# Kernel optimization log

Measured on AMD Instinct MI355X. Metric: run time of the kernel, lower is better.

Reference implementation:

```python
import jax, jax.numpy as jnp
import numpy as np


def gcn_conv(x, W, b, src, dst, dinv_sqrt, n_nodes):
    # PyG GCNConv: h = X W; out_i = sum_j norm_ij * h_j + b, norm = d_i^-1/2 d_j^-1/2
    h = x @ W  # [N, out]
    norm = dinv_sqrt[src] * dinv_sqrt[dst]  # [E]
    msg = h[src] * norm[:, None]  # [E, out]
    out = jax.ops.segment_sum(msg, dst, num_segments=n_nodes)
    return out + b


def setup_inputs() -> dict:
    key = jax.random.key(0)
    ks = jax.random.split(key, 12)
    N, E, G = 50000, 400000, 512
    x = jax.random.normal(ks[0], (N, 3), dtype=jnp.float32)
    edge_index = jax.random.randint(ks[1], (2, E), 0, N, dtype=jnp.int64)
    batch = jnp.sort(jax.random.randint(ks[2], (N,), 0, G, dtype=jnp.int64))
    def lin(k, fin, fout):
        kw, kb = jax.random.split(k)
        s = 1.0 / np.sqrt(fin)
        return (jax.random.uniform(kw, (fin, fout), jnp.float32, -s, s),
                jax.random.uniform(kb, (fout,), jnp.float32, -s, s))
    W1, b1 = lin(ks[3], 3, 100)
    W2, b2 = lin(ks[4], 100, 200)
    W3, b3 = lin(ks[5], 200, 100)
    W4, b4 = lin(ks[6], 100, 1)
    return {"x": x, "edge_index": edge_index, "batch": batch, "num_graphs": G,
            "W1": W1, "b1": b1, "W2": W2, "b2": b2,
            "W3": W3, "b3": b3, "W4": W4, "b4": b4}


def reference(x, edge_index, batch, num_graphs, W1, b1, W2, b2, W3, b3, W4, b4):
    N = x.shape[0]
    loop = jnp.arange(N, dtype=edge_index.dtype)
    src = jnp.concatenate([edge_index[0], loop])  # self-loops added (GCNConv default)
    dst = jnp.concatenate([edge_index[1], loop])
    deg = jax.ops.segment_sum(jnp.ones_like(src, dtype=x.dtype), dst, num_segments=N)
    dinv_sqrt = deg ** -0.5  # deg >= 1 due to self-loops

    h = jax.nn.silu(gcn_conv(x, W1, b1, src, dst, dinv_sqrt, N))
    h = jax.nn.silu(gcn_conv(h, W2, b2, src, dst, dinv_sqrt, N))

    # global_mean_pool over `batch` segments
    sums = jax.ops.segment_sum(h, batch, num_segments=num_graphs)  # [G, 200]
    cnts = jax.ops.segment_sum(jnp.ones((N,), h.dtype), batch, num_segments=num_graphs)
    pooled = sums / jnp.maximum(cnts, 1.0)[:, None]

    h = jax.nn.silu(pooled @ W3 + b3)
    out = h @ W4 + b4  # [G, 1]
    return out.squeeze(-1)
```

## Files before the change

### kernel.cpp

```cpp
#include <hip/hip_runtime.h>
#include <math.h>

#define WF 64

__device__ __forceinline__ float silu_f(float v){
  float e = __builtin_amdgcn_exp2f(v * -1.44269504088896340736f);
  return v * __builtin_amdgcn_rcpf(1.0f + e);
}

typedef __attribute__((ext_vector_type(8))) short bf16x8;
typedef __attribute__((ext_vector_type(4))) float f32x4;

__device__ __forceinline__ void bf16split(float v, unsigned short& h, unsigned short& l){
  unsigned int b = __float_as_uint(v);
  unsigned int hh = (b + 0x8000u) >> 16;
  float hf = __uint_as_float(hh << 16);
  float lo = v - hf;
  unsigned int bl = __float_as_uint(lo);
  h = (unsigned short)hh;
  l = (unsigned short)((bl + 0x8000u) >> 16);
}

__global__ __launch_bounds__(256) void k_count(const int* __restrict__ dst, int* __restrict__ cnt, int E){
  int e = blockIdx.x*blockDim.x + threadIdx.x;
  if (e < E) atomicAdd(&cnt[dst[e]], 1);
}

__global__ __launch_bounds__(256) void k_scan1(const int* __restrict__ cnt, int* __restrict__ rowstart, int* __restrict__ bsum, int N){
  __shared__ int s[256];
  int tid = threadIdx.x;
  int base = blockIdx.x*2048 + tid*8;
  int loc[8]; int tsum = 0;
#pragma unroll
  for (int j=0;j<8;++j){ int idx=base+j; int v = (idx<N)?cnt[idx]:0; loc[j]=tsum; tsum+=v; }
  s[tid]=tsum; __syncthreads();
  for (int off=1; off<256; off<<=1){
    int v = (tid>=off)? s[tid-off] : 0;
    __syncthreads();
    s[tid] += v;
    __syncthreads();
  }
  int texc = s[tid] - tsum;
  if (tid==255) bsum[blockIdx.x] = s[255];
#pragma unroll
  for (int j=0;j<8;++j){ int idx=base+j; if (idx<N) rowstart[idx] = texc + loc[j]; }
}

__global__ __launch_bounds__(256) void k_scan3(const int* __restrict__ bsum, const int* __restrict__ cnt,
                        const float* __restrict__ x,
                        int* __restrict__ rowstart, int* __restrict__ cursor,
                        float4* __restrict__ dxp,
                        int N, int E, int nb){
  __shared__ int boffs;
  int tid = threadIdx.x;
  int b = (blockIdx.x*blockDim.x) >> 11;
  if (tid < WF){
    int v = (tid < nb && tid < b) ? bsum[tid] : 0;
#pragma unroll
    for (int off=32; off; off>>=1) v += __shfl_down(v, off);
    if (tid==0) boffs = v;
  }
  __syncthreads();
  int idx = blockIdx.x*blockDim.x + tid;
  if (idx < N){
    int v = rowstart[idx] + boffs;
    rowstart[idx]=v; cursor[idx]=v;
    float di = rsqrtf((float)(cnt[idx]+1));
    float4 o;
    o.x = di;
    o.y = di*x[3*idx+0];
    o.z = di*x[3*idx+1];
    o.w = di*x[3*idx+2];
    dxp[idx] = o;
  }
  if (idx==0) rowstart[N]=E;
}

__global__ __launch_bounds__(256) void k_fill(const int* __restrict__ src, const int* __restrict__ dst,
                       int* __restrict__ cursor, int* __restrict__ colsrc, int E){
  int e = blockIdx.x*blockDim.x + threadIdx.x;
  if (e < E){
    int d = dst[e];
    int pos = atomicAdd(&cursor[d], 1);
    colsrc[pos] = src[e];
  }
}

__global__ __launch_bounds__(256) void k_wconv(const float* __restrict__ W2,
                       unsigned short* __restrict__ w2th, unsigned short* __restrict__ w2tl){
  int idx = blockIdx.x*blockDim.x + threadIdx.x;
  if (idx < 224*128){
    int f = idx >> 7, k = idx & 127;
    float v = (f < 200 && k < 100) ? W2[(size_t)k*200 + f] : 0.f;
    unsigned short h, l;
    bf16split(v, h, l);
    w2th[idx] = h;
    w2tl[idx] = l;
  }
}

__global__ __launch_bounds__(256) void k_z1(const float4* __restrict__ dxp,
                     const int* __restrict__ rowstart, const int* __restrict__ colsrc,
                     float4* __restrict__ z1, int N){
  int i = blockIdx.x*blockDim.x + threadIdx.x;
  if (i >= N) return;
  float4 self = dxp[i];
  float di = self.x;
  float sx = self.y, sy = self.z, sz = self.w;
  int jb = rowstart[i], je = rowstart[i+1];
  int j = jb;
  for (; j+3 < je; j += 4){
    float4 r0 = dxp[colsrc[j]];
    float4 r1 = dxp[colsrc[j+1]];
    float4 r2 = dxp[colsrc[j+2]];
    float4 r3 = dxp[colsrc[j+3]];
    sx += (r0.y + r1.y) + (r2.y + r3.y);
    sy += (r0.z + r1.z) + (r2.z + r3.z);
    sz += (r0.w + r1.w) + (r2.w + r3.w);
  }
  for (; j < je; ++j){
    float4 r = dxp[colsrc[j]];
    sx += r.y; sy += r.z; sz += r.w;
  }
  float4 o;
  o.x = di;
  o.y = di*sx; o.z = di*sy; o.w = di*sz;
  z1[i] = o;
}

__global__ __launch_bounds__(256) void k_agg2f(const float4* __restrict__ z1,
                       const int* __restrict__ rowstart, const int* __restrict__ colsrc,
                       const float* __restrict__ W1, const float* __restrict__ b1,
                       unsigned short* __restrict__ a2h, unsigned short* __restrict__ a2l, int N){
  __shared__ float w[300];
  __shared__ float bb[100];
  int tid = threadIdx.x;
  for (int t=tid; t<300; t+=256) w[t]=W1[t];
  for (int t=tid; t<100; t+=256) bb[t]=b1[t];
  __syncthreads();

  int node = blockIdx.x*8 + (tid >> 5);
  int lane = tid & 31;
  if (node >= N) return;
  if (lane >= 25){
    int ko = 100 + (lane-25)*4;
    ushort4 z = make_ushort4(0,0,0,0);
    *(ushort4*)(a2h + (size_t)node*128 + ko) = z;
    *(ushort4*)(a2l + (size_t)node*128 + ko) = z;
    return;
  }
  int f0 = lane*4;
  float w0[4], w1[4], w2[4], b[4];
#pragma unroll
  for (int j=0;j<4;++j){
    w0[j] = w[f0+j]; w1[j] = w[100+f0+j]; w2[j] = w[200+f0+j]; b[j] = bb[f0+j];
  }

  float4 zn = z1[node];
  float din = zn.x;
  float acc[4];
#pragma unroll
  for (int j=0;j<4;++j){
    float h = silu_f(zn.y*w0[j] + zn.z*w1[j] + zn.w*w2[j] + b[j]);
    acc[j] = din*h;
  }
  int jb = rowstart[node], je = rowstart[node+1];
  int e = jb;
  for (; e+1 < je; e += 2){
    float4 zu0 = z1[colsrc[e]];
    float4 zu1 = z1[colsrc[e+1]];
#pragma unroll
    for (int j=0;j<4;++j){
      float h0 = silu_f(zu0.y*w0[j] + zu0.z*w1[j] + zu0.w*w2[j] + b[j]);
      float h1v = silu_f(zu1.y*w0[j] + zu1.z*w1[j] + zu1.w*w2[j] + b[j]);
      acc[j] += zu0.x*h0 + zu1.x*h1v;
    }
  }
  if (e < je){
    float4 zu = z1[colsrc[e]];
#pragma unroll
    for (int j=0;j<4;++j){
      float h = silu_f(zu.y*w0[j] + zu.z*w1[j] + zu.w*w2[j] + b[j]);
      acc[j] += zu.x*h;
    }
  }
  ushort4 h4, l4;
  bf16split(din*acc[0], h4.x, l4.x);
  bf16split(din*acc[1], h4.y, l4.y);
  bf16split(din*acc[2], h4.z, l4.z);
  bf16split(din*acc[3], h4.w, l4.w);
  *(ushort4*)(a2h + (size_t)node*128 + f0) = h4;
  *(ushort4*)(a2l + (size_t)node*128 + f0) = l4;
}

__global__ __launch_bounds__(128) void k_mm2(const unsigned short* __restrict__ a2h,
                      const unsigned short* __restrict__ a2l,
                      const unsigned short* __restrict__ w2th,
                      const unsigned short* __restrict__ w2tl,
                      const float* __restrict__ b2, const int* __restrict__ batch,
                      float* __restrict__ pooled, int N, int nwg){
  __shared__ float plL[256];
  int tid = threadIdx.x;
  int l = tid & 63, w = tid >> 6;
  int orig = blockIdx.x;
  int q = nwg >> 3, r = nwg & 7;
  int xcd = orig % 8, rk = orig / 8;
  int bid = (xcd < r) ? (xcd*(q+1) + rk) : (r*(q+1) + (xcd-r)*q + rk);
  int n0 = bid * 32;
  int row = l & 15;
  int kg  = l >> 4;

  const unsigned short* ah_p = a2h + (size_t)(n0 + w*16 + row)*128;
  const unsigned short* al_p = a2l + (size_t)(n0 + w*16 + row)*128;

  bf16x8 ahf[4], alf[4];
#pragma unroll
  for (int ks = 0; ks < 4; ++ks){
    int ko = ks*32 + kg*8;
    ahf[ks] = *(const bf16x8*)(ah_p + ko);
    alf[ks] = *(const bf16x8*)(al_p + ko);
  }

  int g0 = batch[n0];

  for (int fb = 0; fb < 7; ++fb){
    int gf0 = fb*32 + row, gf1 = gf0 + 16;
    const unsigned short* wh0_p = w2th + (size_t)gf0*128;
    const unsigned short* wl0_p = w2tl + (size_t)gf0*128;
    const unsigned short* wh1_p = w2th + (size_t)gf1*128;
    const unsigned short* wl1_p = w2tl + (size_t)gf1*128;

    f32x4 acc0 = {0.f,0.f,0.f,0.f};
    f32x4 acc1 = {0.f,0.f,0.f,0.f};
#pragma unroll
    for (int ks = 0; ks < 4; ++ks){
      int ko = ks*32 + kg*8;
      bf16x8 wh0 = *(const bf16x8*)(wh0_p + ko);
      bf16x8 wl0 = *(const bf16x8*)(wl0_p + ko);
      bf16x8 wh1 = *(const bf16x8*)(wh1_p + ko);
      bf16x8 wl1 = *(const bf16x8*)(wl1_p + ko);
      acc0 = __builtin_amdgcn_mfma_f32_16x16x32_bf16(ahf[ks], wh0, acc0, 0, 0, 0);
      acc0 = __builtin_amdgcn_mfma_f32_16x16x32_bf16(ahf[ks], wl0, acc0, 0, 0, 0);
      acc0 = __builtin_amdgcn_mfma_f32_16x16x32_bf16(alf[ks], wh0, acc0, 0, 0, 0);
      acc1 = __builtin_amdgcn_mfma_f32_16x16x32_bf16(ahf[ks], wh1, acc1, 0, 0, 0);
      acc1 = __builtin_amdgcn_mfma_f32_16x16x32_bf16(ahf[ks], wl1, acc1, 0, 0, 0);
      acc1 = __builtin_amdgcn_mfma_f32_16x16x32_bf16(alf[ks], wh1, acc1, 0, 0, 0);
    }

    __syncthreads();
    for (int idx = tid; idx < 256; idx += 128) plL[idx] = 0.f;
    __syncthreads();

#pragma unroll
    for (int ft = 0; ft < 2; ++ft){
      f32x4 a = ft ? acc1 : acc0;
      int fl = ft*16 + row;
      int gf = fb*32 + fl;
      if (gf < 200){
        float bias = b2[gf];
        float s = 0.f;
        int gprev = -1;
#pragma unroll
        for (int r2 = 0; r2 < 4; ++r2){
          int node = n0 + w*16 + kg*4 + r2;
          if (node < N){
            int g = batch[node];
            if (g != gprev){
              if (gprev >= 0){
                int dg = gprev - g0;
                if (dg < 8) atomicAdd(&plL[dg*32 + fl], s);
                else        atomicAdd(&pooled[(size_t)gprev*200 + gf], s);
              }
              gprev = g; s = 0.f;
            }
            s += silu_f(a[r2] + bias);
          }
        }
        if (gprev >= 0){
          int dg = gprev - g0;
          if (dg < 8) atomicAdd(&plL[dg*32 + fl], s);
          else        atomicAdd(&pooled[(size_t)gprev*200 + gf], s);
        }
      }
    }
    __syncthreads();
    for (int idx = tid; idx < 256; idx += 128){
      float v = plL[idx];
      if (v != 0.f){
        int r2 = idx >> 5, f = idx & 31;
        int gf = fb*32 + f;
        if (gf < 200) atomicAdd(&pooled[(size_t)(g0+r2)*200 + gf], v);
      }
    }
  }
}

__global__ __launch_bounds__(256) void k_head(const float* __restrict__ pooled, const int* __restrict__ batch,
                       const float* __restrict__ W3, const float* __restrict__ b3,
                       const float* __restrict__ W4, const float* __restrict__ b4,
                       float* __restrict__ out, int N){
  __shared__ float pl[200];
  __shared__ float h3[100];
  int g = blockIdx.x; int tid = threadIdx.x;
  int lo=0, hi=N;
  while (lo<hi){ int m=(lo+hi)>>1; if (batch[m] < g) lo=m+1; else hi=m; }
  int s = lo;
  hi=N;
  while (lo<hi){ int m=(lo+hi)>>1; if (batch[m] < g+1) lo=m+1; else hi=m; }
  int e = lo;
  float inv = (e>s) ? 1.0f/(float)(e-s) : 0.0f;
  if (tid < 200) pl[tid] = pooled[(size_t)g*200 + tid] * inv;
  __syncthreads();
  if (tid < 100){
    float acc = b3[tid];
    for (int k=0;k<200;++k) acc += pl[k]*W3[k*100+tid];
    h3[tid] = silu_f(acc);
  }
  __syncthreads();
  if (tid < WF){
    float p = 0.f;
    if (tid < 100)      p  = h3[tid]     * W4[tid];
    if (tid + 64 < 100) p += h3[tid+64]  * W4[tid+64];
#pragma unroll
    for (int off=32; off; off>>=1) p += __shfl_down(p, off);
    if (tid==0) out[g] = p + b4[0];
  }
}

extern "C" void kernel_launch(void* const* d_in, const int* in_sizes, int n_in,
                              void* d_out, int out_size, void* d_ws, size_t ws_size,
                              hipStream_t stream){
  const float* x  = (const float*)d_in[0];
  const int*   ei = (const int*)  d_in[1];
  const int* batch= (const int*)  d_in[2];
  const float* W1 = (const float*)d_in[4];
  const float* b1 = (const float*)d_in[5];
  const float* W2 = (const float*)d_in[6];
  const float* b2 = (const float*)d_in[7];
  const float* W3 = (const float*)d_in[8];
  const float* b3 = (const float*)d_in[9];
  const float* W4 = (const float*)d_in[10];
  const float* b4 = (const float*)d_in[11];
  float* out = (float*)d_out;

  int N = in_sizes[0]/3;
  int E = in_sizes[1]/2;
  int G = out_size;
  const int* src = ei;
  const int* dst = ei + E;
  int NP = ((N + 63)/64)*64;

  char* base = (char*)d_ws; size_t off = 0;
  auto alloc = [&](size_t bytes)->void*{
    void* p = base + off;
    off = (off + bytes + 255) & ~(size_t)255;
    return p;
  };
  int*   cnt      = (int*)  alloc((size_t)N*4);
  float* pooled   = (float*)alloc((size_t)G*200*4);
  size_t zbytes   = off;
  int*   rowstart = (int*)  alloc((size_t)(N+1)*4);
  int*   cursor   = (int*)  alloc((size_t)N*4);
  int*   bsum     = (int*)  alloc(4096);
  int*   colsrc   = (int*)  alloc((size_t)E*4);
  float4* dxp     = (float4*)alloc((size_t)N*16);
  float4* z1      = (float4*)alloc((size_t)N*16);
  unsigned short* a2h = (unsigned short*)alloc((size_t)NP*128*2);
  unsigned short* a2l = (unsigned short*)alloc((size_t)NP*128*2);
  unsigned short* w2th = (unsigned short*)alloc((size_t)224*128*2);
  unsigned short* w2tl = (unsigned short*)alloc((size_t)224*128*2);
  (void)ws_size; (void)n_in;

  hipMemsetAsync(base, 0, zbytes, stream);
  int gE = (E+255)/256;
  k_count<<<gE,256,0,stream>>>(dst, cnt, E);
  int nb = (N+2047)/2048;
  k_scan1<<<nb,256,0,stream>>>(cnt, rowstart, bsum, N);
  k_scan3<<<(N+255)/256,256,0,stream>>>(bsum, cnt, x, rowstart, cursor, dxp, N, E, nb);
  k_wconv<<<(224*128+255)/256,256,0,stream>>>(W2, w2th, w2tl);
  k_fill<<<gE,256,0,stream>>>(src, dst, cursor, colsrc, E);
  k_z1<<<(N+255)/256,256,0,stream>>>(dxp, rowstart, colsrc, z1, N);
  k_agg2f<<<(N+7)/8,256,0,stream>>>(z1, rowstart, colsrc, W1, b1, a2h, a2l, N);
  int nwg = (N+31)/32;
  k_mm2<<<nwg,128,0,stream>>>(a2h, a2l, w2th, w2tl, b2, batch, pooled, N, nwg);
  k_head<<<G,256,0,stream>>>(pooled, batch, W3, b3, W4, b4, out, N);
}
```

Measured before the change: 179.1 us.

## Fuse weight conversion into count kernel, unroll gather, prefetch weights in mm2

Merges the W2 bf16 split-conversion kernel into the edge-count kernel as extra blocks, removing one launch. The layer-2 aggregation loop is unrolled from 2 to 4 neighbors so more gathers are in flight. In the MMA pooling kernel, batch ids are loaded once, the first k-slice of the next weight block is prefetched into registers, and the shared-memory pool buffer is cleared during the readback, which drops one barrier per feature block. These changes add register pressure in the gather and MMA kernels.

```diff
diff --git a/kernel.cpp b/kernel.cpp
--- a/kernel.cpp
+++ b/kernel.cpp
@@ -21,9 +21,25 @@
   l = (unsigned short)((bl + 0x8000u) >> 16);
 }
 
-__global__ __launch_bounds__(256) void k_count(const int* __restrict__ dst, int* __restrict__ cnt, int E){
-  int e = blockIdx.x*blockDim.x + threadIdx.x;
-  if (e < E) atomicAdd(&cnt[dst[e]], 1);
+__global__ __launch_bounds__(256) void k_count_wconv(const int* __restrict__ dst, int* __restrict__ cnt, int E,
+                       const float* __restrict__ W2,
+                       unsigned short* __restrict__ w2th, unsigned short* __restrict__ w2tl,
+                       int nCountBlocks){
+  int b = blockIdx.x;
+  if (b < nCountBlocks){
+    int e = b*256 + threadIdx.x;
+    if (e < E) atomicAdd(&cnt[dst[e]], 1);
+  } else {
+    int idx = (b - nCountBlocks)*256 + threadIdx.x;
+    if (idx < 224*128){
+      int f = idx >> 7, k = idx & 127;
+      float v = (f < 200 && k < 100) ? W2[(size_t)k*200 + f] : 0.f;
+      unsigned short h, l;
+      bf16split(v, h, l);
+      w2th[idx] = h;
+      w2tl[idx] = l;
+    }
+  }
 }
 
 __global__ __launch_bounds__(256) void k_scan1(const int* __restrict__ cnt, int* __restrict__ rowstart, int* __restrict__ bsum, int N){
@@ -83,19 +99,6 @@
     int d = dst[e];
     int pos = atomicAdd(&cursor[d], 1);
     colsrc[pos] = src[e];
-  }
-}
-
-__global__ __launch_bounds__(256) void k_wconv(const float* __restrict__ W2,
-                       unsigned short* __restrict__ w2th, unsigned short* __restrict__ w2tl){
-  int idx = blockIdx.x*blockDim.x + threadIdx.x;
-  if (idx < 224*128){
-    int f = idx >> 7, k = idx & 127;
-    float v = (f < 200 && k < 100) ? W2[(size_t)k*200 + f] : 0.f;
-    unsigned short h, l;
-    bf16split(v, h, l);
-    w2th[idx] = h;
-    w2tl[idx] = l;
   }
 }
 
@@ -166,17 +169,21 @@
   }
   int jb = rowstart[node], je = rowstart[node+1];
   int e = jb;
-  for (; e+1 < je; e += 2){
+  for (; e+3 < je; e += 4){
     float4 zu0 = z1[colsrc[e]];
     float4 zu1 = z1[colsrc[e+1]];
+    float4 zu2 = z1[colsrc[e+2]];
+    float4 zu3 = z1[colsrc[e+3]];
 #pragma unroll
     for (int j=0;j<4;++j){
       float h0 = silu_f(zu0.y*w0[j] + zu0.z*w1[j] + zu0.w*w2[j] + b[j]);
       float h1v = silu_f(zu1.y*w0[j] + zu1.z*w1[j] + zu1.w*w2[j] + b[j]);
-      acc[j] += zu0.x*h0 + zu1.x*h1v;
-    }
-  }
-  if (e < je){
+      float h2v = silu_f(zu2.y*w0[j] + zu2.z*w1[j] + zu2.w*w2[j] + b[j]);
+      float h3v = silu_f(zu3.y*w0[j] + zu3.z*w1[j] + zu3.w*w2[j] + b[j]);
+      acc[j] += (zu0.x*h0 + zu1.x*h1v) + (zu2.x*h2v + zu3.x*h3v);
+    }
+  }
+  for (; e < je; ++e){
     float4 zu = z1[colsrc[e]];
 #pragma unroll
     for (int j=0;j<4;++j){
@@ -222,6 +229,20 @@
   }
 
   int g0 = batch[n0];
+  int nodebatch[4];
+#pragma unroll
+  for (int r2 = 0; r2 < 4; ++r2){
+    int node = n0 + w*16 + kg*4 + r2;
+    nodebatch[r2] = (node < N) ? batch[node] : -1;
+  }
+
+  for (int idx = tid; idx < 256; idx += 128) plL[idx] = 0.f;
+
+  int kof = kg*8;
+  bf16x8 pwh0 = *(const bf16x8*)(w2th + (size_t)(row     )*128 + kof);
+  bf16x8 pwl0 = *(const bf16x8*)(w2tl + (size_t)(row     )*128 + kof);
+  bf16x8 pwh1 = *(const bf16x8*)(w2th + (size_t)(16 + row)*128 + kof);
+  bf16x8 pwl1 = *(const bf16x8*)(w2tl + (size_t)(16 + row)*128 + kof);
 
   for (int fb = 0; fb < 7; ++fb){
     int gf0 = fb*32 + row, gf1 = gf0 + 16;
@@ -232,8 +253,14 @@
 
     f32x4 acc0 = {0.f,0.f,0.f,0.f};
     f32x4 acc1 = {0.f,0.f,0.f,0.f};
-#pragma unroll
-    for (int ks = 0; ks < 4; ++ks){
+    acc0 = __builtin_amdgcn_mfma_f32_16x16x32_bf16(ahf[0], pwh0, acc0, 0, 0, 0);
+    acc0 = __builtin_amdgcn_mfma_f32_16x16x32_bf16(ahf[0], pwl0, acc0, 0, 0, 0);
+    acc0 = __builtin_amdgcn_mfma_f32_16x16x32_bf16(alf[0], pwh0, acc0, 0, 0, 0);
+    acc1 = __builtin_amdgcn_mfma_f32_16x16x32_bf16(ahf[0], pwh1, acc1, 0, 0, 0);
+    acc1 = __builtin_amdgcn_mfma_f32_16x16x32_bf16(ahf[0], pwl1, acc1, 0, 0, 0);
+    acc1 = __builtin_amdgcn_mfma_f32_16x16x32_bf16(alf[0], pwh1, acc1, 0, 0, 0);
+#pragma unroll
+    for (int ks = 1; ks < 4; ++ks){
       int ko = ks*32 + kg*8;
       bf16x8 wh0 = *(const bf16x8*)(wh0_p + ko);
       bf16x8 wl0 = *(const bf16x8*)(wl0_p + ko);
@@ -247,10 +274,15 @@
       acc1 = __builtin_amdgcn_mfma_f32_16x16x32_bf16(alf[ks], wh1, acc1, 0, 0, 0);
     }
 
+    if (fb < 6){
+      int ngf0 = (fb+1)*32 + row, ngf1 = ngf0 + 16;
+      pwh0 = *(const bf16x8*)(w2th + (size_t)ngf0*128 + kof);
+      pwl0 = *(const bf16x8*)(w2tl + (size_t)ngf0*128 + kof);
+      pwh1 = *(const bf16x8*)(w2th + (size_t)ngf1*128 + kof);
+      pwl1 = *(const bf16x8*)(w2tl + (size_t)ngf1*128 + kof);
+    }
+
     __syncthreads();
-    for (int idx = tid; idx < 256; idx += 128) plL[idx] = 0.f;
-    __syncthreads();
-
 #pragma unroll
     for (int ft = 0; ft < 2; ++ft){
       f32x4 a = ft ? acc1 : acc0;
@@ -262,9 +294,8 @@
         int gprev = -1;
 #pragma unroll
         for (int r2 = 0; r2 < 4; ++r2){
-          int node = n0 + w*16 + kg*4 + r2;
-          if (node < N){
-            int g = batch[node];
+          int g = nodebatch[r2];
+          if (g >= 0){
             if (g != gprev){
               if (gprev >= 0){
                 int dg = gprev - g0;
@@ -286,6 +317,7 @@
     __syncthreads();
     for (int idx = tid; idx < 256; idx += 128){
       float v = plL[idx];
+      plL[idx] = 0.f;
       if (v != 0.f){
         int r2 = idx >> 5, f = idx & 31;
         int gf = fb*32 + f;
@@ -373,11 +405,11 @@
 
   hipMemsetAsync(base, 0, zbytes, stream);
   int gE = (E+255)/256;
-  k_count<<<gE,256,0,stream>>>(dst, cnt, E);
+  int gW = (224*128+255)/256;
+  k_count_wconv<<<gE+gW,256,0,stream>>>(dst, cnt, E, W2, w2th, w2tl, gE);
   int nb = (N+2047)/2048;
   k_scan1<<<nb,256,0,stream>>>(cnt, rowstart, bsum, N);
   k_scan3<<<(N+255)/256,256,0,stream>>>(bsum, cnt, x, rowstart, cursor, dxp, N, E, nb);
-  k_wconv<<<(224*128+255)/256,256,0,stream>>>(W2, w2th, w2tl);
   k_fill<<<gE,256,0,stream>>>(src, dst, cursor, colsrc, E);
   k_z1<<<(N+255)/256,256,0,stream>>>(dxp, rowstart, colsrc, z1, N);
   k_agg2f<<<(N+7)/8,256,0,stream>>>(z1, rowstart, colsrc, W1, b1, a2h, a2l, N);
```

After: 169.2 us. -5.5%, faster.
